# Optimization experiments

Hardware: AMD Instinct MI355X
Metric: run time of the kernel (lower is better)

## Reference

```python
import jax, jax.numpy as jnp
import numpy as np

N, M, D = 131072, 128, 128

def setup_inputs() -> dict:
    key = jax.random.key(0)
    k1, k2, k3 = jax.random.split(key, 3)
    X = jax.random.normal(k1, (N, D), dtype=jnp.float32)
    r = jax.random.uniform(k2, (N, M), dtype=jnp.float32)
    mus = jax.random.normal(k3, (M, D), dtype=jnp.float32)
    return {"X": X, "r": r, "mus": mus}

def reference(X, r, mus):
    # Squared pairwise L2 distances without materializing [N, M, D]:
    x2 = jnp.sum(X * X, axis=1)            # [N]
    mu2 = jnp.sum(mus * mus, axis=1)       # [M]
    cross = X @ mus.T                      # [N, M]
    dist2 = jnp.maximum(x2[:, None] + mu2[None, :] - 2.0 * cross, 0.0)
    loss = jnp.sum(r * dist2) / X.shape[0]
    return loss
```

## Files before the change

kernel.cpp:

```cpp
#include <hip/hip_runtime.h>
#include <hip/hip_bf16.h>


typedef __attribute__((ext_vector_type(8)))  short  short8;
typedef __attribute__((ext_vector_type(16))) float  float16v;

__device__ __forceinline__ unsigned short f32_bf16(float f) {
    unsigned int u = __float_as_uint(f);
    u += 0x7fffu + ((u >> 16) & 1u);
    return (unsigned short)(u >> 16);
}

__global__ void zero_out_kernel(float* out) { out[0] = 0.0f; }

__global__ __launch_bounds__(256, 4)
void isoloss_kernel(const float* __restrict__ X,
                    const float* __restrict__ r,
                    const float* __restrict__ mus,
                    float* __restrict__ out)
{
    const int tid  = threadIdx.x;
    const int wave = tid >> 6;
    const int lane = tid & 63;
    const int col  = lane & 31;
    const int half = lane >> 5;

    __shared__ unsigned short ldsA[32][136];
    __shared__ float x2s[32];
    __shared__ float wsum[4];

    short8 bfrag[8];
    float mu2p = 0.0f;
    {
        const float* mrow = mus + (size_t)(wave * 32 + col) * 128;
        #pragma unroll
        for (int ks = 0; ks < 8; ++ks) {
            const float4 a = *(const float4*)(mrow + ks * 16 + half * 8);
            const float4 b = *(const float4*)(mrow + ks * 16 + half * 8 + 4);
            mu2p += a.x*a.x + a.y*a.y + a.z*a.z + a.w*a.w
                  + b.x*b.x + b.y*b.y + b.z*b.z + b.w*b.w;
            short8 f;
            f[0] = (short)f32_bf16(a.x); f[1] = (short)f32_bf16(a.y);
            f[2] = (short)f32_bf16(a.z); f[3] = (short)f32_bf16(a.w);
            f[4] = (short)f32_bf16(b.x); f[5] = (short)f32_bf16(b.y);
            f[6] = (short)f32_bf16(b.z); f[7] = (short)f32_bf16(b.w);
            bfrag[ks] = f;
        }
    }
    const float mu2 = mu2p + __shfl_xor(mu2p, 32);

    float s = 0.0f;

    const int row_stage = tid >> 3;
    const int c0        = (tid & 7) * 4;

    for (int g = blockIdx.x; g < 4096; g += gridDim.x) {
        const int rowbase = g * 32;

        __syncthreads();

        {
            const float* xrow = X + (size_t)(rowbase + row_stage) * 128;
            float p = 0.0f;
            #pragma unroll
            for (int j = 0; j < 4; ++j) {
                const float4 v = *(const float4*)(xrow + c0 + j * 32);
                p += v.x*v.x + v.y*v.y + v.z*v.z + v.w*v.w;
                ushort4 h;
                h.x = f32_bf16(v.x); h.y = f32_bf16(v.y);
                h.z = f32_bf16(v.z); h.w = f32_bf16(v.w);
                *(ushort4*)&ldsA[row_stage][c0 + j * 32] = h;
            }
            p += __shfl_down(p, 4);
            p += __shfl_down(p, 2);
            p += __shfl_down(p, 1);
            if ((tid & 7) == 0) x2s[row_stage] = p;
        }
        __syncthreads();

        float16v acc = {};
        #pragma unroll
        for (int ks = 0; ks < 8; ++ks) {
            const short8 af = *(const short8*)&ldsA[col][ks * 16 + half * 8];
            acc = __builtin_amdgcn_mfma_f32_32x32x16_bf16(af, bfrag[ks], acc, 0, 0, 0);
        }

        const float* rbase = r + (size_t)rowbase * 128 + wave * 32 + col;
        #pragma unroll
        for (int reg = 0; reg < 16; ++reg) {
            const int rl = (reg & 3) + 8 * (reg >> 2) + 4 * half;
            float d = x2s[rl] + mu2 - 2.0f * acc[reg];
            d = fmaxf(d, 0.0f);
            s += rbase[(size_t)rl * 128] * d;
        }
    }

    #pragma unroll
    for (int off = 32; off > 0; off >>= 1) s += __shfl_down(s, off);
    if (lane == 0) wsum[wave] = s;
    __syncthreads();
    if (tid == 0) {
        const float t = wsum[0] + wsum[1] + wsum[2] + wsum[3];
        atomicAdd(out, t * (1.0f / 131072.0f));
    }
}

extern "C" void kernel_launch(void* const* d_in, const int* in_sizes, int n_in,
                              void* d_out, int out_size, void* d_ws, size_t ws_size,
                              hipStream_t stream) {
    const float* X   = (const float*)d_in[0];
    const float* r   = (const float*)d_in[1];
    const float* mus = (const float*)d_in[2];
    float* out = (float*)d_out;

    zero_out_kernel<<<1, 1, 0, stream>>>(out);
    isoloss_kernel<<<1024, 256, 0, stream>>>(X, r, mus, out);
}
```

Before: 159.9 us.

## Load X directly into MFMA fragments, dropping LDS staging and barriers

Each wave now loads its own X rows straight from global memory, converts them to bf16 in registers and feeds the MFMA, instead of staging through shared memory with two block barriers per tile. Row norms are computed in registers and broadcast with shuffles, and r values are prefetched before the matmul to overlap their latency. Conversion uses a packed bf16 builtin when available. The cost is that all four waves redundantly read the same X tile, relying on cache hits.

New measurement: 171.8 us. +7.5%, slower.

```diff
diff --git a/kernel.cpp b/kernel.cpp
--- a/kernel.cpp
+++ b/kernel.cpp
@@ -5,10 +5,24 @@
 typedef __attribute__((ext_vector_type(8)))  short  short8;
 typedef __attribute__((ext_vector_type(16))) float  float16v;
 
-__device__ __forceinline__ unsigned short f32_bf16(float f) {
-    unsigned int u = __float_as_uint(f);
-    u += 0x7fffu + ((u >> 16) & 1u);
-    return (unsigned short)(u >> 16);
+#if defined(__has_builtin)
+#if __has_builtin(__builtin_amdgcn_cvt_pk_bf16_f32)
+#define HAVE_PK_BF16 1
+#endif
+#endif
+
+__device__ __forceinline__ unsigned int pk_bf16(float x, float y) {
+#ifdef HAVE_PK_BF16
+    typedef __attribute__((ext_vector_type(2))) __bf16 bf16x2;
+    bf16x2 p = __builtin_amdgcn_cvt_pk_bf16_f32(x, y);
+    return __builtin_bit_cast(unsigned int, p);
+#else
+    unsigned int ux = __float_as_uint(x);
+    unsigned int uy = __float_as_uint(y);
+    ux += 0x7fffu + ((ux >> 16) & 1u);
+    uy += 0x7fffu + ((uy >> 16) & 1u);
+    return (ux >> 16) | (uy & 0xffff0000u);
+#endif
 }
 
 __global__ void zero_out_kernel(float* out) { out[0] = 0.0f; }
@@ -25,73 +39,65 @@
     const int col  = lane & 31;
     const int half = lane >> 5;
 
-    __shared__ unsigned short ldsA[32][136];
-    __shared__ float x2s[32];
     __shared__ float wsum[4];
 
     short8 bfrag[8];
     float mu2p = 0.0f;
     {
-        const float* mrow = mus + (size_t)(wave * 32 + col) * 128;
+        const float* mrow = mus + (size_t)(wave * 32 + col) * 128 + half * 8;
         #pragma unroll
         for (int ks = 0; ks < 8; ++ks) {
-            const float4 a = *(const float4*)(mrow + ks * 16 + half * 8);
-            const float4 b = *(const float4*)(mrow + ks * 16 + half * 8 + 4);
+            const float4 a = *(const float4*)(mrow + ks * 16);
+            const float4 b = *(const float4*)(mrow + ks * 16 + 4);
             mu2p += a.x*a.x + a.y*a.y + a.z*a.z + a.w*a.w
                   + b.x*b.x + b.y*b.y + b.z*b.z + b.w*b.w;
-            short8 f;
-            f[0] = (short)f32_bf16(a.x); f[1] = (short)f32_bf16(a.y);
-            f[2] = (short)f32_bf16(a.z); f[3] = (short)f32_bf16(a.w);
-            f[4] = (short)f32_bf16(b.x); f[5] = (short)f32_bf16(b.y);
-            f[6] = (short)f32_bf16(b.z); f[7] = (short)f32_bf16(b.w);
-            bfrag[ks] = f;
+            union { short8 s8; uint4 u4; } u;
+            u.u4.x = pk_bf16(a.x, a.y);
+            u.u4.y = pk_bf16(a.z, a.w);
+            u.u4.z = pk_bf16(b.x, b.y);
+            u.u4.w = pk_bf16(b.z, b.w);
+            bfrag[ks] = u.s8;
         }
     }
     const float mu2 = mu2p + __shfl_xor(mu2p, 32);
 
     float s = 0.0f;
 
-    const int row_stage = tid >> 3;
-    const int c0        = (tid & 7) * 4;
-
     for (int g = blockIdx.x; g < 4096; g += gridDim.x) {
         const int rowbase = g * 32;
+        const float* xp = X + (size_t)(rowbase + col) * 128 + half * 8;
+        const float* rp = r + (size_t)rowbase * 128 + wave * 32 + col;
 
-        __syncthreads();
-
-        {
-            const float* xrow = X + (size_t)(rowbase + row_stage) * 128;
-            float p = 0.0f;
-            #pragma unroll
-            for (int j = 0; j < 4; ++j) {
-                const float4 v = *(const float4*)(xrow + c0 + j * 32);
-                p += v.x*v.x + v.y*v.y + v.z*v.z + v.w*v.w;
-                ushort4 h;
-                h.x = f32_bf16(v.x); h.y = f32_bf16(v.y);
-                h.z = f32_bf16(v.z); h.w = f32_bf16(v.w);
-                *(ushort4*)&ldsA[row_stage][c0 + j * 32] = h;
-            }
-            p += __shfl_down(p, 4);
-            p += __shfl_down(p, 2);
-            p += __shfl_down(p, 1);
-            if ((tid & 7) == 0) x2s[row_stage] = p;
-        }
-        __syncthreads();
-
-        float16v acc = {};
-        #pragma unroll
-        for (int ks = 0; ks < 8; ++ks) {
-            const short8 af = *(const short8*)&ldsA[col][ks * 16 + half * 8];
-            acc = __builtin_amdgcn_mfma_f32_32x32x16_bf16(af, bfrag[ks], acc, 0, 0, 0);
-        }
-
-        const float* rbase = r + (size_t)rowbase * 128 + wave * 32 + col;
+        float rv[16];
         #pragma unroll
         for (int reg = 0; reg < 16; ++reg) {
             const int rl = (reg & 3) + 8 * (reg >> 2) + 4 * half;
-            float d = x2s[rl] + mu2 - 2.0f * acc[reg];
-            d = fmaxf(d, 0.0f);
-            s += rbase[(size_t)rl * 128] * d;
+            rv[reg] = rp[(size_t)rl * 128];
+        }
+
+        float16v acc = {};
+        float p = 0.0f;
+        #pragma unroll
+        for (int ks = 0; ks < 8; ++ks) {
+            const float4 a = *(const float4*)(xp + ks * 16);
+            const float4 b = *(const float4*)(xp + ks * 16 + 4);
+            p += a.x*a.x + a.y*a.y + a.z*a.z + a.w*a.w
+               + b.x*b.x + b.y*b.y + b.z*b.z + b.w*b.w;
+            union { short8 s8; uint4 u4; } u;
+            u.u4.x = pk_bf16(a.x, a.y);
+            u.u4.y = pk_bf16(a.z, a.w);
+            u.u4.z = pk_bf16(b.x, b.y);
+            u.u4.w = pk_bf16(b.z, b.w);
+            acc = __builtin_amdgcn_mfma_f32_32x32x16_bf16(u.s8, bfrag[ks], acc, 0, 0, 0);
+        }
+        const float x2v = p + __shfl_xor(p, 32);
+
+        #pragma unroll
+        for (int reg = 0; reg < 16; ++reg) {
+            const int rl = (reg & 3) + 8 * (reg >> 2) + 4 * half;
+            const float x2r = __shfl(x2v, rl);
+            float d = fmaxf(x2r + mu2 - 2.0f * acc[reg], 0.0f);
+            s += rv[reg] * d;
         }
     }
 
```
